# Kernel optimization log

Measured on AMD Instinct MI355X. Metric: run time of the kernel, lower is better.

Reference implementation:

```python
import jax, jax.numpy as jnp
import numpy as np

B = 1024        # number of graphs
MAXLEN = 64     # max nodes per graph (pad_sequence length)
E = 256         # hidden_size
H = 8           # num_heads
HD = E // H     # head dim
NEG = -1e9


def setup_inputs() -> dict:
    key = jax.random.key(0)
    k0, k1, k2 = jax.random.split(key, 3)
    lens = np.tile(np.array([32, 48, 64, 40], dtype=np.int64), B // 4)  # sum = 47104
    batch_indices = jnp.asarray(np.repeat(np.arange(B, dtype=np.int64), lens))
    N = int(lens.sum())
    node_features = jax.random.normal(k0, (N, E), dtype=jnp.float32)
    in_proj_w = jax.random.normal(k1, (3 * E, E), dtype=jnp.float32) * (1.0 / np.sqrt(E))
    in_proj_b = jnp.zeros((3 * E,), dtype=jnp.float32)
    out_proj_w = jax.random.normal(k2, (E, E), dtype=jnp.float32) * (1.0 / np.sqrt(E))
    out_proj_b = jnp.zeros((E,), dtype=jnp.float32)
    return {"node_features": node_features, "batch_indices": batch_indices,
            "in_proj_w": in_proj_w, "in_proj_b": in_proj_b,
            "out_proj_w": out_proj_w, "out_proj_b": out_proj_b}


def _pad_ragged(node_features, batch_indices):
    # counts per graph, start offset of each graph, position of each node in its graph
    N = node_features.shape[0]
    counts = jax.ops.segment_sum(jnp.ones((N,), jnp.int32), batch_indices, num_segments=B)
    starts = jnp.cumsum(counts) - counts
    pos = jnp.arange(N) - starts[batch_indices]
    padded = jnp.zeros((B, MAXLEN, E), node_features.dtype).at[batch_indices, pos].set(node_features)
    key_pad = jnp.arange(MAXLEN)[None, :] >= counts[:, None]  # [B, L] True = padding
    return padded, key_pad


def reference(node_features, batch_indices, in_proj_w, in_proj_b, out_proj_w, out_proj_b):
    padded, key_pad = _pad_ragged(node_features, batch_indices)   # [B,L,E], [B,L]
    qkv = padded @ in_proj_w.T + in_proj_b                        # [B,L,3E]
    q, k, v = jnp.split(qkv, 3, axis=-1)
    q = q.reshape(B, MAXLEN, H, HD)
    k = k.reshape(B, MAXLEN, H, HD)
    v = v.reshape(B, MAXLEN, H, HD)
    scores = jnp.einsum('blhd,bmhd->bhlm', q, k) / jnp.sqrt(jnp.float32(HD))
    scores = jnp.where(key_pad[:, None, None, :], NEG, scores)    # mask padded keys
    attn = jax.nn.softmax(scores, axis=-1)                        # [B,H,L,L]
    ctx = jnp.einsum('bhlm,bmhd->blhd', attn, v).reshape(B, MAXLEN, E)
    out = ctx @ out_proj_w.T + out_proj_b                         # [B,L,E]
    out = jnp.transpose(out, (1, 0, 2))                           # [L,B,E] seq-first like torch
    weights = attn.mean(axis=1)                                   # [B,L,L] head-averaged
    return out, weights
```

## Files before the change

### kernel.cpp

```cpp
#include <hip/hip_runtime.h>

typedef unsigned short u16;
typedef short bf16x8 __attribute__((ext_vector_type(8)));
typedef float f32x4 __attribute__((ext_vector_type(4)));

#define MFMA16(a, b, c) __builtin_amdgcn_mfma_f32_16x16x32_bf16((a), (b), (c), 0, 0, 0)

static __device__ __forceinline__ u16 f2bf(float f) {
    union { float f; unsigned int u; } v; v.f = f;
    unsigned int u = v.u;
    u += 0x7fffu + ((u >> 16) & 1u);
    return (u16)(u >> 16);
}

__global__ void prep_kernel(const int* __restrict__ bidx, int N,
                            const float* __restrict__ w_in, const float* __restrict__ w_out,
                            int* __restrict__ starts, int* __restrict__ counts,
                            u16* __restrict__ w_in_bf, u16* __restrict__ w_out_bf) {
    int tid = blockIdx.x * blockDim.x + threadIdx.x;
    if (tid < 1024) {
        int lo = 0, hi = N;
        while (lo < hi) { int mid = (lo + hi) >> 1; if (bidx[mid] < tid) lo = mid + 1; else hi = mid; }
        int s0 = lo;
        lo = 0; hi = N;
        int v1 = tid + 1;
        while (lo < hi) { int mid = (lo + hi) >> 1; if (bidx[mid] < v1) lo = mid + 1; else hi = mid; }
        starts[tid] = s0;
        counts[tid] = lo - s0;
    }
    {
        float4 v = ((const float4*)w_in)[tid];
        ushort4 o; o.x = f2bf(v.x); o.y = f2bf(v.y); o.z = f2bf(v.z); o.w = f2bf(v.w);
        ((ushort4*)w_in_bf)[tid] = o;
    }
    if (tid < 16384) {
        float4 v = ((const float4*)w_out)[tid];
        ushort4 o; o.x = f2bf(v.x); o.y = f2bf(v.y); o.z = f2bf(v.z); o.w = f2bf(v.w);
        ((ushort4*)w_out_bf)[tid] = o;
    }
}

__global__ __launch_bounds__(512, 2) void gat_kernel(
    const float* __restrict__ X, const float* __restrict__ bias_in,
    const float* __restrict__ bias_out,
    const int* __restrict__ starts, const int* __restrict__ counts,
    const u16* __restrict__ w_in_bf, const u16* __restrict__ w_out_bf,
    float* __restrict__ out, float* __restrict__ wout) {

    __shared__ u16 qg[64][72];
    __shared__ u16 kg[64][72];
    __shared__ u16 vt[64][72];
    __shared__ u16 p_s[8][16][72];
    __shared__ u16 cs[64][264];

    const int b = blockIdx.x;
    const int tid = threadIdx.x;
    const int w = tid >> 6;
    const int lane = tid & 63;
    const int n = lane & 15;
    const int quad = lane >> 4;
    const int s = starts[b];
    const int c = counts[b];

    const int wh = w >> 2;
    const int wj = w & 3;
    const int hh = w & 1;
    const int rt = w >> 1;
    const int m0 = rt * 16;

    bf16x8 afr[2][8];
    #pragma unroll
    for (int st2 = 0; st2 < 2; ++st2) {
        int row = wh * 32 + st2 * 16 + n;
        bool ok = row < c;
        const float* src = X + (long)(s + row) * 256 + quad * 8;
        #pragma unroll
        for (int ks = 0; ks < 8; ++ks) {
            float4 v0 = make_float4(0.f, 0.f, 0.f, 0.f);
            float4 v1 = make_float4(0.f, 0.f, 0.f, 0.f);
            if (ok) {
                v0 = *(const float4*)(src + ks * 32);
                v1 = *(const float4*)(src + ks * 32 + 4);
            }
            bf16x8 a;
            a[0] = (short)f2bf(v0.x); a[1] = (short)f2bf(v0.y);
            a[2] = (short)f2bf(v0.z); a[3] = (short)f2bf(v0.w);
            a[4] = (short)f2bf(v1.x); a[5] = (short)f2bf(v1.y);
            a[6] = (short)f2bf(v1.z); a[7] = (short)f2bf(v1.w);
            afr[st2][ks] = a;
        }
    }

    const float scale = 0.17677669529663687f;
    float wacc[4][4];
    #pragma unroll
    for (int t = 0; t < 4; ++t)
        #pragma unroll
        for (int r = 0; r < 4; ++r) wacc[t][r] = 0.f;

    #pragma unroll 1
    for (int g = 0; g < 4; ++g) {
        #pragma unroll
        for (int i = 0; i < 3; ++i) {
            const int wrow = i * 256 + g * 64 + wj * 16 + n;
            const u16* wr = w_in_bf + wrow * 256 + quad * 8;
            const float bias = bias_in[wrow];

            f32x4 acc[2];
            acc[0] = (f32x4){0.f, 0.f, 0.f, 0.f};
            acc[1] = (f32x4){0.f, 0.f, 0.f, 0.f};
            #pragma unroll
            for (int kh = 0; kh < 2; ++kh) {
                bf16x8 bfr[4];
                #pragma unroll
                for (int k4 = 0; k4 < 4; ++k4) bfr[k4] = *(const bf16x8*)(wr + (kh * 4 + k4) * 32);
                #pragma unroll
                for (int k4 = 0; k4 < 4; ++k4) {
                    acc[0] = MFMA16(afr[0][kh * 4 + k4], bfr[k4], acc[0]);
                    acc[1] = MFMA16(afr[1][kh * 4 + k4], bfr[k4], acc[1]);
                }
            }

            #pragma unroll
            for (int st2 = 0; st2 < 2; ++st2) {
                const int st = 2 * wh + st2;
                if (i == 2) {
                    ushort4 pk;
                    pk.x = f2bf(acc[st2][0] + bias); pk.y = f2bf(acc[st2][1] + bias);
                    pk.z = f2bf(acc[st2][2] + bias); pk.w = f2bf(acc[st2][3] + bias);
                    *(ushort4*)&vt[wj * 16 + n][st * 16 + quad * 4] = pk;
                } else {
                    u16 (*dst)[72] = i ? kg : qg;
                    #pragma unroll
                    for (int r = 0; r < 4; ++r)
                        dst[st * 16 + quad * 4 + r][wj * 16 + n] = f2bf(acc[st2][r] + bias);
                }
            }
        }
        __syncthreads();

        {
            const int h = g * 2 + hh;
            bf16x8 aq = *(const bf16x8*)&qg[m0 + n][hh * 32 + quad * 8];
            f32x4 sc[4];
            #pragma unroll
            for (int t = 0; t < 4; ++t) {
                bf16x8 bk = *(const bf16x8*)&kg[t * 16 + n][hh * 32 + quad * 8];
                f32x4 z = (f32x4){0.f, 0.f, 0.f, 0.f};
                sc[t] = MFMA16(aq, bk, z);
            }
            float p[4][4], inv[4];
            #pragma unroll
            for (int r = 0; r < 4; ++r) {
                float mx = -1e30f;
                #pragma unroll
                for (int t = 0; t < 4; ++t) {
                    float sv = ((t * 16 + n) < c) ? sc[t][r] * scale : -1e30f;
                    p[t][r] = sv;
                    mx = fmaxf(mx, sv);
                }
                #pragma unroll
                for (int d = 1; d < 16; d <<= 1) mx = fmaxf(mx, __shfl_xor(mx, d, 64));
                float sm = 0.f;
                #pragma unroll
                for (int t = 0; t < 4; ++t) {
                    float e = ((t * 16 + n) < c) ? __expf(p[t][r] - mx) : 0.f;
                    p[t][r] = e; sm += e;
                }
                #pragma unroll
                for (int d = 1; d < 16; d <<= 1) sm += __shfl_xor(sm, d, 64);
                inv[r] = 1.f / sm;
                #pragma unroll
                for (int t = 0; t < 4; ++t) wacc[t][r] += p[t][r] * (inv[r] * 0.125f);
            }
            #pragma unroll
            for (int t = 0; t < 4; ++t)
                #pragma unroll
                for (int r = 0; r < 4; ++r)
                    p_s[w][quad * 4 + r][t * 16 + n] = f2bf(p[t][r]);
            #pragma unroll
            for (int nt = 0; nt < 2; ++nt) {
                f32x4 acc = (f32x4){0.f, 0.f, 0.f, 0.f};
                #pragma unroll
                for (int k2 = 0; k2 < 2; ++k2) {
                    bf16x8 ap = *(const bf16x8*)&p_s[w][n][k2 * 32 + quad * 8];
                    bf16x8 bv = *(const bf16x8*)&vt[hh * 32 + nt * 16 + n][k2 * 32 + quad * 8];
                    acc = MFMA16(ap, bv, acc);
                }
                #pragma unroll
                for (int r = 0; r < 4; ++r)
                    cs[m0 + quad * 4 + r][h * 32 + nt * 16 + n] = f2bf(acc[r] * inv[r]);
            }
        }
        __syncthreads();
    }

    {
        float* pw = (float*)&p_s[w & ~1][0][0];
        if (hh == 0) {
            #pragma unroll
            for (int t = 0; t < 4; ++t)
                #pragma unroll
                for (int r = 0; r < 4; ++r)
                    pw[(quad * 4 + r) * 64 + t * 16 + n] = wacc[t][r];
        }
        __syncthreads();
        if (hh == 1) {
            #pragma unroll
            for (int t = 0; t < 4; ++t)
                #pragma unroll
                for (int r = 0; r < 4; ++r)
                    wout[b * 4096 + (m0 + quad * 4 + r) * 64 + t * 16 + n] =
                        wacc[t][r] + pw[(quad * 4 + r) * 64 + t * 16 + n];
        }
    }

    {
        const int sp = w & 1;
        const int cq = w >> 1;
        bf16x8 actx[2][8];
        #pragma unroll
        for (int st2 = 0; st2 < 2; ++st2)
            #pragma unroll
            for (int ks = 0; ks < 8; ++ks)
                actx[st2][ks] = *(const bf16x8*)&cs[(2 * sp + st2) * 16 + n][ks * 32 + quad * 8];

        #pragma unroll 2
        for (int ci = 0; ci < 4; ++ci) {
            const int ct = 4 * cq + ci;
            const u16* wr = w_out_bf + (ct * 16 + n) * 256 + quad * 8;
            f32x4 acc[2];
            acc[0] = (f32x4){0.f, 0.f, 0.f, 0.f};
            acc[1] = (f32x4){0.f, 0.f, 0.f, 0.f};
            #pragma unroll
            for (int kh = 0; kh < 2; ++kh) {
                bf16x8 bfr[4];
                #pragma unroll
                for (int k4 = 0; k4 < 4; ++k4) bfr[k4] = *(const bf16x8*)(wr + (kh * 4 + k4) * 32);
                #pragma unroll
                for (int k4 = 0; k4 < 4; ++k4) {
                    acc[0] = MFMA16(actx[0][kh * 4 + k4], bfr[k4], acc[0]);
                    acc[1] = MFMA16(actx[1][kh * 4 + k4], bfr[k4], acc[1]);
                }
            }
            float bias = bias_out[ct * 16 + n];
            #pragma unroll
            for (int st2 = 0; st2 < 2; ++st2) {
                const int orow = (2 * sp + st2) * 16 + quad * 4;
                #pragma unroll
                for (int r = 0; r < 4; ++r)
                    out[(orow + r) * 262144 + b * 256 + ct * 16 + n] = acc[st2][r] + bias;
            }
        }
    }
}

extern "C" void kernel_launch(void* const* d_in, const int* in_sizes, int n_in,
                              void* d_out, int out_size, void* d_ws, size_t ws_size,
                              hipStream_t stream) {
    const float* X     = (const float*)d_in[0];
    const int*   bidx  = (const int*)d_in[1];
    const float* w_in  = (const float*)d_in[2];
    const float* b_in  = (const float*)d_in[3];
    const float* w_out = (const float*)d_in[4];
    const float* b_out = (const float*)d_in[5];
    const int N = in_sizes[1];

    float* out  = (float*)d_out;
    float* wout = out + 64 * 1024 * 256;

    int* starts   = (int*)d_ws;
    int* counts   = starts + 1024;
    u16* w_in_bf  = (u16*)(counts + 1024);
    u16* w_out_bf = w_in_bf + 196608;

    hipLaunchKernelGGL(prep_kernel, dim3(192), dim3(256), 0, stream,
                       bidx, N, w_in, w_out, starts, counts, w_in_bf, w_out_bf);
    hipLaunchKernelGGL(gat_kernel, dim3(1024), dim3(512), 0, stream,
                       X, b_in, b_out, starts, counts, w_in_bf, w_out_bf, out, wout);
}
```

Before: 293.7 us.

## Transpose score MFMA for in-lane softmax, raise occupancy target, vectorize stores

The score MFMA now has its operands swapped, so each lane holds a full key column per query. The softmax max and sum then need only two cross-lane shuffles, and probabilities are normalised before the PV product. Probability and head-averaged weight writes use packed ushort4/float4 stores. The launch bounds minimum-blocks hint goes from 2 to 4, the QKV inner loop is no longer unrolled, and the padding on the ctx LDS buffer is removed. Together these aim to cut shuffle and store overhead and raise occupancy, but they risk register spills from the tighter register budget and LDS bank conflicts on the unpadded buffer.

```diff
diff --git a/kernel.cpp b/kernel.cpp
--- a/kernel.cpp
+++ b/kernel.cpp
@@ -40,7 +40,7 @@
     }
 }
 
-__global__ __launch_bounds__(512, 2) void gat_kernel(
+__global__ __launch_bounds__(512, 4) void gat_kernel(
     const float* __restrict__ X, const float* __restrict__ bias_in,
     const float* __restrict__ bias_out,
     const int* __restrict__ starts, const int* __restrict__ counts,
@@ -51,7 +51,7 @@
     __shared__ u16 kg[64][72];
     __shared__ u16 vt[64][72];
     __shared__ u16 p_s[8][16][72];
-    __shared__ u16 cs[64][264];
+    __shared__ u16 cs[64][256];
 
     const int b = blockIdx.x;
     const int tid = threadIdx.x;
@@ -100,7 +100,7 @@
 
     #pragma unroll 1
     for (int g = 0; g < 4; ++g) {
-        #pragma unroll
+        #pragma unroll 1
         for (int i = 0; i < 3; ++i) {
             const int wrow = i * 256 + g * 64 + wj * 16 + n;
             const u16* wr = w_in_bf + wrow * 256 + quad * 8;
@@ -147,37 +147,45 @@
             for (int t = 0; t < 4; ++t) {
                 bf16x8 bk = *(const bf16x8*)&kg[t * 16 + n][hh * 32 + quad * 8];
                 f32x4 z = (f32x4){0.f, 0.f, 0.f, 0.f};
-                sc[t] = MFMA16(aq, bk, z);
-            }
-            float p[4][4], inv[4];
-            #pragma unroll
-            for (int r = 0; r < 4; ++r) {
-                float mx = -1e30f;
-                #pragma unroll
-                for (int t = 0; t < 4; ++t) {
-                    float sv = ((t * 16 + n) < c) ? sc[t][r] * scale : -1e30f;
-                    p[t][r] = sv;
+                sc[t] = MFMA16(bk, aq, z);
+            }
+            float pv[4][4];
+            float mx = -1e30f;
+            #pragma unroll
+            for (int t = 0; t < 4; ++t)
+                #pragma unroll
+                for (int r = 0; r < 4; ++r) {
+                    float sv = ((t * 16 + quad * 4 + r) < c) ? sc[t][r] * scale : -1e30f;
+                    pv[t][r] = sv;
                     mx = fmaxf(mx, sv);
                 }
-                #pragma unroll
-                for (int d = 1; d < 16; d <<= 1) mx = fmaxf(mx, __shfl_xor(mx, d, 64));
-                float sm = 0.f;
-                #pragma unroll
-                for (int t = 0; t < 4; ++t) {
-                    float e = ((t * 16 + n) < c) ? __expf(p[t][r] - mx) : 0.f;
-                    p[t][r] = e; sm += e;
-                }
-                #pragma unroll
-                for (int d = 1; d < 16; d <<= 1) sm += __shfl_xor(sm, d, 64);
-                inv[r] = 1.f / sm;
-                #pragma unroll
-                for (int t = 0; t < 4; ++t) wacc[t][r] += p[t][r] * (inv[r] * 0.125f);
-            }
+            mx = fmaxf(mx, __shfl_xor(mx, 16, 64));
+            mx = fmaxf(mx, __shfl_xor(mx, 32, 64));
+            float sm = 0.f;
             #pragma unroll
             for (int t = 0; t < 4; ++t)
                 #pragma unroll
-                for (int r = 0; r < 4; ++r)
-                    p_s[w][quad * 4 + r][t * 16 + n] = f2bf(p[t][r]);
+                for (int r = 0; r < 4; ++r) {
+                    float e = ((t * 16 + quad * 4 + r) < c) ? __expf(pv[t][r] - mx) : 0.f;
+                    pv[t][r] = e; sm += e;
+                }
+            sm += __shfl_xor(sm, 16, 64);
+            sm += __shfl_xor(sm, 32, 64);
+            float invs = 1.f / sm;
+            #pragma unroll
+            for (int t = 0; t < 4; ++t)
+                #pragma unroll
+                for (int r = 0; r < 4; ++r) {
+                    pv[t][r] *= invs;
+                    wacc[t][r] += pv[t][r] * 0.125f;
+                }
+            #pragma unroll
+            for (int t = 0; t < 4; ++t) {
+                ushort4 pk;
+                pk.x = f2bf(pv[t][0]); pk.y = f2bf(pv[t][1]);
+                pk.z = f2bf(pv[t][2]); pk.w = f2bf(pv[t][3]);
+                *(ushort4*)&p_s[w][n][t * 16 + quad * 4] = pk;
+            }
             #pragma unroll
             for (int nt = 0; nt < 2; ++nt) {
                 f32x4 acc = (f32x4){0.f, 0.f, 0.f, 0.f};
@@ -189,7 +197,7 @@
                 }
                 #pragma unroll
                 for (int r = 0; r < 4; ++r)
-                    cs[m0 + quad * 4 + r][h * 32 + nt * 16 + n] = f2bf(acc[r] * inv[r]);
+                    cs[m0 + quad * 4 + r][h * 32 + nt * 16 + n] = f2bf(acc[r]);
             }
         }
         __syncthreads();
@@ -199,19 +207,21 @@
         float* pw = (float*)&p_s[w & ~1][0][0];
         if (hh == 0) {
             #pragma unroll
-            for (int t = 0; t < 4; ++t)
-                #pragma unroll
-                for (int r = 0; r < 4; ++r)
-                    pw[(quad * 4 + r) * 64 + t * 16 + n] = wacc[t][r];
+            for (int t = 0; t < 4; ++t) {
+                float4 f4 = make_float4(wacc[t][0], wacc[t][1], wacc[t][2], wacc[t][3]);
+                *(float4*)&pw[n * 72 + t * 16 + quad * 4] = f4;
+            }
         }
         __syncthreads();
         if (hh == 1) {
             #pragma unroll
-            for (int t = 0; t < 4; ++t)
-                #pragma unroll
-                for (int r = 0; r < 4; ++r)
-                    wout[b * 4096 + (m0 + quad * 4 + r) * 64 + t * 16 + n] =
-                        wacc[t][r] + pw[(quad * 4 + r) * 64 + t * 16 + n];
+            for (int t = 0; t < 4; ++t) {
+                float4 f4 = *(const float4*)&pw[n * 72 + t * 16 + quad * 4];
+                float4 o;
+                o.x = wacc[t][0] + f4.x; o.y = wacc[t][1] + f4.y;
+                o.z = wacc[t][2] + f4.z; o.w = wacc[t][3] + f4.w;
+                *(float4*)&wout[b * 4096 + (m0 + n) * 64 + t * 16 + quad * 4] = o;
+            }
         }
     }
 
```

Result: no change. 288.0 us (-1.9%).
